# Kernel optimization log

Hardware: AMD Instinct MI355X
Metric: run time of the kernel (lower is better)

Reference implementation:

```python
import jax, jax.numpy as jnp
import numpy as np

B, S, D = 4, 2048, 1024
ATTN_D, OUT_D, H = 1024, 1024, 16
EPS = 1e-12


def setup_inputs() -> dict:
    key = jax.random.key(0)
    ks = jax.random.split(key, 9)
    s = 0.02
    return {
        "x": jax.random.normal(ks[0], (B, S, D), dtype=jnp.float32),
        "wq": jax.random.normal(ks[1], (D, ATTN_D), dtype=jnp.float32) * s,
        "bq": jnp.zeros((ATTN_D,), dtype=jnp.float32),
        "wk": jax.random.normal(ks[2], (D, ATTN_D), dtype=jnp.float32) * s,
        "bk": jnp.zeros((ATTN_D,), dtype=jnp.float32),
        "wv": jax.random.normal(ks[3], (D, ATTN_D), dtype=jnp.float32) * s,
        "bv": jnp.zeros((ATTN_D,), dtype=jnp.float32),
        "wo": jax.random.normal(ks[4], (ATTN_D, OUT_D), dtype=jnp.float32) * s,
        "bo": jnp.zeros((OUT_D,), dtype=jnp.float32),
        "ln_g": jnp.ones((OUT_D,), dtype=jnp.float32),
        "ln_b": jnp.zeros((OUT_D,), dtype=jnp.float32),
    }


def reference(x, wq, bq, wk, bk, wv, bv, wo, bo, ln_g, ln_b):
    b, s, _ = x.shape
    hd = ATTN_D // H  # head_dim
    # projections -> [B, H, S, hd]
    q = (x @ wq + bq).reshape(b, s, H, hd).transpose(0, 2, 1, 3)
    k = (x @ wk + bk).reshape(b, s, H, hd).transpose(0, 2, 1, 3)
    v = (x @ wv + bv).reshape(b, s, H, hd).transpose(0, 2, 1, 3)
    # full O(S^2) score matrix, as in the original module
    scores = jnp.einsum("bhqd,bhkd->bhqk", q, k) / jnp.sqrt(jnp.float32(hd))
    attn = jax.nn.softmax(scores, axis=-1)
    out = jnp.einsum("bhqk,bhkd->bhqd", attn, v)
    out = out.transpose(0, 2, 1, 3).reshape(b, s, ATTN_D)
    out = out @ wo + bo
    # LayerNorm (no residual in this module)
    mu = jnp.mean(out, axis=-1, keepdims=True)
    var = jnp.var(out, axis=-1, keepdims=True)
    out = (out - mu) * jax.lax.rsqrt(var + EPS) * ln_g + ln_b
    return out
```

## Files before the change

### kernel.cpp

```cpp
#include <hip/hip_runtime.h>

typedef __bf16 bf16;
typedef __bf16 bf16x4 __attribute__((ext_vector_type(4)));
typedef __bf16 bf16x8 __attribute__((ext_vector_type(8)));
typedef float f32x4 __attribute__((ext_vector_type(4)));

#define NB 4
#define NS 2048
#define ND 1024
#define NH 16
#define HD 64

#define QSCALE 0.18033688f

__device__ __forceinline__ void gload_lds16(const void* g, void* l) {
  __builtin_amdgcn_global_load_lds(
      (const __attribute__((address_space(1))) void*)g,
      (__attribute__((address_space(3))) void*)l, 16, 0, 0);
}

__device__ __forceinline__ float fast_exp2(float x) {
#if __has_builtin(__builtin_amdgcn_exp2f)
  return __builtin_amdgcn_exp2f(x);
#else
  return exp2f(x);
#endif
}

__global__ __launch_bounds__(256) void k_cvt(const float* __restrict__ src,
                                             bf16* __restrict__ dst) {
  size_t i = ((size_t)blockIdx.x * 256 + threadIdx.x) * 4;
  float4 v = *(const float4*)(src + i);
  bf16x4 o = {(__bf16)v.x, (__bf16)v.y, (__bf16)v.z, (__bf16)v.w};
  *(bf16x4*)(dst + i) = o;
}

__global__ __launch_bounds__(256) void k_cvt_T4(const float* __restrict__ wq,
                                                const float* __restrict__ wk,
                                                const float* __restrict__ wv,
                                                const float* __restrict__ wo,
                                                bf16* __restrict__ wqkvT,
                                                bf16* __restrict__ woT) {
  int z = blockIdx.z;
  const float* src = z == 0 ? wq : z == 1 ? wk : z == 2 ? wv : wo;
  bf16* dst = z < 3 ? wqkvT + (size_t)z * 1048576 : woT;
  __shared__ float t[32][33];
  int tx = threadIdx.x, ty = threadIdx.y;
  int x = blockIdx.x * 32 + tx;
  int y = blockIdx.y * 32 + ty;
#pragma unroll
  for (int j = 0; j < 4; ++j)
    t[ty + j * 8][tx] = src[(size_t)(y + j * 8) * 1024 + x];
  __syncthreads();
  int x2 = blockIdx.y * 32 + tx;
  int y2 = blockIdx.x * 32 + ty;
#pragma unroll
  for (int j = 0; j < 4; ++j)
    dst[(size_t)(y2 + j * 8) * 1024 + x2] = (__bf16)t[tx][ty + j * 8];
}

__global__ __launch_bounds__(256) void k_vT(const bf16* __restrict__ V,
                                            bf16* __restrict__ Vt) {
  __shared__ bf16 t[64][72];
  int tid = threadIdx.x;
  int bh = blockIdx.x >> 5, st = blockIdx.x & 31;
  int b = bh >> 4, h = bh & 15;
  const bf16* src = V + ((size_t)b * NS + st * 64) * ND + h * HD;
#pragma unroll
  for (int rep = 0; rep < 2; ++rep) {
    int idx = rep * 256 + tid;
    int r = idx >> 3, c8 = (idx & 7) * 8;
    *(bf16x8*)&t[r][c8] = *(const bf16x8*)(src + (size_t)r * ND + c8);
  }
  __syncthreads();
  bf16* dst = Vt + (size_t)bh * HD * NS + st * 64;
#pragma unroll
  for (int rep = 0; rep < 2; ++rep) {
    int idx = rep * 256 + tid;
    int d = idx >> 3, s8 = (idx & 7) * 8;
    bf16x8 v;
#pragma unroll
    for (int j = 0; j < 8; ++j) {
      int jj = (j + tid) & 7;
      v[jj] = t[s8 + jj][d];
    }
    *(bf16x8*)(dst + (size_t)d * NS + s8) = v;
  }
}

__device__ __forceinline__ void gemm256_mainloop(const bf16* __restrict__ A,
                                                 const bf16* __restrict__ BT,
                                                 int bm, int bn, bf16* As,
                                                 bf16* Bs, f32x4 acc[4][4]) {
  const int tid = threadIdx.x;
  const int w = tid >> 6, lane = tid & 63, quad = lane >> 4, l15 = lane & 15;
  const int l7 = l15 & 7, l8 = lane >> 3;
  const int wr = w >> 1, wc = w & 1;
  const int gsw = ((lane & 7) ^ l8) * 8;
  const bf16* gaw = A + (size_t)(bm * 256 + w * 8 + l8) * 1024 + gsw;
  const bf16* gbw = BT + (size_t)(bn * 128 + w * 8 + l8) * 1024 + gsw;
  bf16* daw = As + w * 512;
  bf16* dbw = Bs + w * 512;
  int aoff[4][2], boff[4][2];
#pragma unroll
  for (int mi = 0; mi < 4; ++mi)
#pragma unroll
    for (int ks = 0; ks < 2; ++ks)
      aoff[mi][ks] =
          (wr * 64 + mi * 16 + l15) * 64 + (((ks * 4 + quad) ^ l7) * 8);
#pragma unroll
  for (int ni = 0; ni < 4; ++ni)
#pragma unroll
    for (int ks = 0; ks < 2; ++ks)
      boff[ni][ks] =
          (wc * 64 + ni * 16 + l15) * 64 + (((ks * 4 + quad) ^ l7) * 8);

  auto stage = [&](int kt) {
    const int slot = kt % 3;
    const bf16* ga = gaw + kt * 64;
    const bf16* gb = gbw + kt * 64;
    bf16* da = daw + slot * 16384;
    bf16* db = dbw + slot * 8192;
#pragma unroll
    for (int ri = 0; ri < 4; ++ri)
      gload_lds16(ga + (size_t)(ri * 64) * 1024, da + ri * 4096);
#pragma unroll
    for (int ri = 0; ri < 2; ++ri)
      gload_lds16(gb + (size_t)(ri * 64) * 1024, db + ri * 4096);
  };

  stage(0);
  stage(1);
  asm volatile("s_waitcnt vmcnt(6)" ::: "memory");
  __builtin_amdgcn_s_barrier();

  for (int kt = 0; kt < 16; ++kt) {
    const int slot = kt % 3;
    if (kt + 2 < 16) stage(kt + 2);
    const bf16* a_ = As + slot * 16384;
    const bf16* b_ = Bs + slot * 8192;
    bf16x8 av[2][2], bv[4][2];
#pragma unroll
    for (int mi = 0; mi < 2; ++mi)
#pragma unroll
      for (int ks = 0; ks < 2; ++ks)
        av[mi][ks] = *(const bf16x8*)(a_ + aoff[mi][ks]);
#pragma unroll
    for (int ni = 0; ni < 4; ++ni)
#pragma unroll
      for (int ks = 0; ks < 2; ++ks)
        bv[ni][ks] = *(const bf16x8*)(b_ + boff[ni][ks]);
    __builtin_amdgcn_s_setprio(1);
#pragma unroll
    for (int mi = 0; mi < 2; ++mi)
#pragma unroll
      for (int ni = 0; ni < 4; ++ni)
#pragma unroll
        for (int ks = 0; ks < 2; ++ks)
          acc[mi][ni] = __builtin_amdgcn_mfma_f32_16x16x32_bf16(
              av[mi][ks], bv[ni][ks], acc[mi][ni], 0, 0, 0);
    __builtin_amdgcn_s_setprio(0);
    bf16x8 av2[2][2];
#pragma unroll
    for (int mi = 0; mi < 2; ++mi)
#pragma unroll
      for (int ks = 0; ks < 2; ++ks)
        av2[mi][ks] = *(const bf16x8*)(a_ + aoff[2 + mi][ks]);
    __builtin_amdgcn_s_setprio(1);
#pragma unroll
    for (int mi = 0; mi < 2; ++mi)
#pragma unroll
      for (int ni = 0; ni < 4; ++ni)
#pragma unroll
        for (int ks = 0; ks < 2; ++ks)
          acc[2 + mi][ni] = __builtin_amdgcn_mfma_f32_16x16x32_bf16(
              av2[mi][ks], bv[ni][ks], acc[2 + mi][ni], 0, 0, 0);
    __builtin_amdgcn_s_setprio(0);
    if (kt + 2 < 16)
      asm volatile("s_waitcnt vmcnt(6)" ::: "memory");
    else
      asm volatile("s_waitcnt vmcnt(0)" ::: "memory");
    if (kt + 1 < 16) __builtin_amdgcn_s_barrier();
  }
  __syncthreads();
}

__global__ __launch_bounds__(512, 2) void k_gemm_qkv(
    const bf16* __restrict__ A, const bf16* __restrict__ BT,
    const float* __restrict__ bq, const float* __restrict__ bk,
    const float* __restrict__ bv, bf16* __restrict__ Q, bf16* __restrict__ K,
    bf16* __restrict__ V) {
  __shared__ alignas(16) char smem[147456];
  bf16* As = (bf16*)smem;
  bf16* Bs = (bf16*)(smem + 98304);
  f32x4 acc[4][4] = {};
  const int bm = blockIdx.y, bn = blockIdx.x;
  gemm256_mainloop(A, BT, bm, bn, As, Bs, acc);
  const int tid = threadIdx.x;
  const int w = tid >> 6, lane = tid & 63, quad = lane >> 4, l15 = lane & 15;
  const int wr = w >> 1, wc = w & 1;
  bf16* sEw = (bf16*)smem + w * 4608;
  const int colbase = bn * 128 + wc * 64;
  const int which = colbase >> 10;
  const int nnbase = colbase & 1023;
  const float* bias = which == 0 ? bq : which == 1 ? bk : bv;
  bf16* dst = which == 0 ? Q : which == 1 ? K : V;
  const float scl = which == 0 ? QSCALE : 1.f;
  const int rowbase = bm * 256 + wr * 64;
#pragma unroll
  for (int ni = 0; ni < 4; ++ni) {
    float bb = bias[nnbase + ni * 16 + l15];
#pragma unroll
    for (int mi = 0; mi < 4; ++mi)
#pragma unroll
      for (int r = 0; r < 4; ++r)
        sEw[(mi * 16 + quad * 4 + r) * 72 + ni * 16 + l15] =
            (__bf16)((acc[mi][ni][r] + bb) * scl);
  }
  const int l8 = lane >> 3, g8 = (lane & 7) * 8;
#pragma unroll
  for (int i = 0; i < 8; ++i) {
    int row = i * 8 + l8;
    bf16x8 vv = *(const bf16x8*)(sEw + row * 72 + g8);
    *(bf16x8*)(dst + (size_t)(rowbase + row) * 1024 + nnbase + g8) = vv;
  }
}

__global__ __launch_bounds__(512, 2) void k_gemm_out(const bf16* __restrict__ A,
                                                     const bf16* __restrict__ BT,
                                                     const float* __restrict__ bo,
                                                     float* __restrict__ Y) {
  __shared__ alignas(16) char smem[147456];
  bf16* As = (bf16*)smem;
  bf16* Bs = (bf16*)(smem + 98304);
  f32x4 acc[4][4] = {};
  const int bm = blockIdx.y, bn = blockIdx.x;
  gemm256_mainloop(A, BT, bm, bn, As, Bs, acc);
  const int tid = threadIdx.x;
  const int w = tid >> 6, lane = tid & 63, quad = lane >> 4, l15 = lane & 15;
  const int wr = w >> 1, wc = w & 1;
  float* sEw = (float*)smem + w * 2176;
  const int colbase = bn * 128 + wc * 64;
  const int rowbase = bm * 256 + wr * 64;
  float bb[4];
#pragma unroll
  for (int ni = 0; ni < 4; ++ni) bb[ni] = bo[colbase + ni * 16 + l15];
  const int l4 = lane >> 4, c4 = (lane & 15) * 4;
#pragma unroll
  for (int h2 = 0; h2 < 2; ++h2) {
#pragma unroll
    for (int ml = 0; ml < 2; ++ml)
#pragma unroll
      for (int ni = 0; ni < 4; ++ni)
#pragma unroll
        for (int r = 0; r < 4; ++r)
          sEw[(ml * 16 + quad * 4 + r) * 68 + ni * 16 + l15] =
              acc[h2 * 2 + ml][ni][r] + bb[ni];
#pragma unroll
    for (int i = 0; i < 8; ++i) {
      int row = i * 4 + l4;
      float4 v = *(const float4*)(sEw + row * 68 + c4);
      *(float4*)(Y + (size_t)(rowbase + h2 * 32 + row) * 1024 + colbase + c4) =
          v;
    }
  }
}

__global__ __launch_bounds__(256, 4) void k_attn(const bf16* __restrict__ Qg,
                                                 const bf16* __restrict__ Kg,
                                                 const bf16* __restrict__ VtG,
                                                 bf16* __restrict__ O) {
  __shared__ alignas(16) char smem[40960];
  bf16* sK = (bf16*)smem;
  bf16* sVt = (bf16*)(smem + 16384);
  const int tid = threadIdx.x;
  const int w = tid >> 6, lane = tid & 63, quad = lane >> 4, l15 = lane & 15;
  const int l7 = l15 & 7, l8 = lane >> 3;
  const int sw = (l15 >> 1) & 3;
  const int bh = blockIdx.x & 63;
  const int qt = blockIdx.x >> 6;
  const int b = bh >> 4, h = bh & 15;
  const bf16* Qh = Qg + (size_t)b * NS * ND + h * HD;
  const bf16* Kh = Kg + (size_t)b * NS * ND + h * HD;
  const bf16* Vh = VtG + (size_t)bh * HD * NS;
  bf16* Pw = (bf16*)(smem + 32768) + w * 1024;

  const int q0 = qt * 128 + w * 32;
  bf16x8 qb[2][2];
#pragma unroll
  for (int ni = 0; ni < 2; ++ni)
#pragma unroll
    for (int ks = 0; ks < 2; ++ks)
      qb[ni][ks] = *(const bf16x8*)(Qh + (size_t)(q0 + ni * 16 + l15) * ND +
                                    ks * 32 + quad * 8);

  const int gsw = ((lane & 7) ^ l8) * 8;
  const bf16* gk = Kh + (size_t)(w * 8 + l8) * ND + gsw;
  const bf16* gv = Vh + (size_t)(w * 8 + l8) * NS + gsw;
  bf16* dk = sK + w * 512;
  bf16* dv = sVt + w * 512;

  f32x4 o_acc[4][2] = {};
  float l_run[2] = {0.f, 0.f};

  int offA[4][2];
#pragma unroll
  for (int mi = 0; mi < 4; ++mi)
#pragma unroll
    for (int ks = 0; ks < 2; ++ks)
      offA[mi][ks] = (mi * 16 + l15) * 64 + (((ks * 4 + quad) ^ l7) * 8);
  int offP[2], wbase[2], wg[2];
#pragma unroll
  for (int ni = 0; ni < 2; ++ni) {
    offP[ni] = (ni * 16 + l15) * 32 + ((quad ^ sw) * 8);
    wbase[ni] = (ni * 16 + l15) * 32 + (quad & 1) * 4;
  }
#pragma unroll
  for (int m2 = 0; m2 < 2; ++m2)
    wg[m2] = (((m2 * 2 + (quad >> 1)) ^ sw) * 8);

  gload_lds16(gk, dk);
  gload_lds16(gk + 32 * ND, dk + 2048);
  gload_lds16(gv, dv);
  gload_lds16(gv + 32 * NS, dv + 2048);

  for (int it = 0; it < NS / 64; ++it) {
    const int buf = (it & 1) * 4096;
    __syncthreads();
    if (it + 1 < NS / 64) {
      const int nbuf = 4096 - buf;
      const bf16* gk1 = gk + (size_t)(it + 1) * 64 * ND;
      const bf16* gv1 = gv + (it + 1) * 64;
      gload_lds16(gk1, dk + nbuf);
      gload_lds16(gk1 + 32 * ND, dk + nbuf + 2048);
      gload_lds16(gv1, dv + nbuf);
      gload_lds16(gv1 + 32 * NS, dv + nbuf + 2048);
    }

#pragma unroll
    for (int hf = 0; hf < 2; ++hf) {
#pragma unroll
      for (int m2 = 0; m2 < 2; ++m2) {
        const int mi = 2 * hf + m2;
        f32x4 s[2] = {};
#pragma unroll
        for (int ks = 0; ks < 2; ++ks) {
          bf16x8 ak = *(const bf16x8*)(sK + buf + offA[mi][ks]);
#pragma unroll
          for (int ni = 0; ni < 2; ++ni)
            s[ni] = __builtin_amdgcn_mfma_f32_16x16x32_bf16(ak, qb[ni][ks],
                                                            s[ni], 0, 0, 0);
        }
#pragma unroll
        for (int ni = 0; ni < 2; ++ni) {
#pragma unroll
          for (int r = 0; r < 4; ++r) {
            s[ni][r] = fast_exp2(s[ni][r]);
            l_run[ni] += s[ni][r];
          }
          bf16x4 p = {(__bf16)s[ni][0], (__bf16)s[ni][1], (__bf16)s[ni][2],
                      (__bf16)s[ni][3]};
          *(bf16x4*)(Pw + wbase[ni] + wg[m2]) = p;
        }
      }

      bf16x8 pb[2];
#pragma unroll
      for (int ni = 0; ni < 2; ++ni)
        pb[ni] = *(const bf16x8*)(Pw + offP[ni]);
#pragma unroll
      for (int mi = 0; mi < 4; ++mi) {
        bf16x8 av = *(const bf16x8*)(sVt + buf + offA[mi][hf]);
#pragma unroll
        for (int ni = 0; ni < 2; ++ni)
          o_acc[mi][ni] = __builtin_amdgcn_mfma_f32_16x16x32_bf16(
              av, pb[ni], o_acc[mi][ni], 0, 0, 0);
      }
    }
  }

#pragma unroll
  for (int ni = 0; ni < 2; ++ni) {
    float l = l_run[ni];
    l += __shfl_xor(l, 16, 64);
    l += __shfl_xor(l, 32, 64);
    float inv = 1.f / l;
    int q = q0 + ni * 16 + l15;
    size_t orow = ((size_t)b * NS + q) * 1024 + h * 64;
#pragma unroll
    for (int mi = 0; mi < 4; ++mi) {
      bf16x4 ov = {
          (__bf16)(o_acc[mi][ni][0] * inv), (__bf16)(o_acc[mi][ni][1] * inv),
          (__bf16)(o_acc[mi][ni][2] * inv), (__bf16)(o_acc[mi][ni][3] * inv)};
      *(bf16x4*)(O + orow + mi * 16 + quad * 4) = ov;
    }
  }
}

__global__ __launch_bounds__(256) void k_ln(float* __restrict__ Y,
                                            const float* __restrict__ g,
                                            const float* __restrict__ bta) {
  int row = blockIdx.x, tid = threadIdx.x;
  float4 v = ((const float4*)(Y + (size_t)row * 1024))[tid];
  float sm = v.x + v.y + v.z + v.w;
  float sq = v.x * v.x + v.y * v.y + v.z * v.z + v.w * v.w;
#pragma unroll
  for (int off = 1; off < 64; off <<= 1) {
    sm += __shfl_xor(sm, off, 64);
    sq += __shfl_xor(sq, off, 64);
  }
  __shared__ float red[8];
  int w = tid >> 6, lane = tid & 63;
  if (lane == 0) {
    red[w] = sm;
    red[4 + w] = sq;
  }
  __syncthreads();
  sm = red[0] + red[1] + red[2] + red[3];
  sq = red[4] + red[5] + red[6] + red[7];
  float mu = sm * (1.f / 1024.f);
  float var = sq * (1.f / 1024.f) - mu * mu;
  float rstd = rsqrtf(var + 1e-12f);
  float4 g4 = ((const float4*)g)[tid];
  float4 b4 = ((const float4*)bta)[tid];
  float4 o;
  o.x = (v.x - mu) * rstd * g4.x + b4.x;
  o.y = (v.y - mu) * rstd * g4.y + b4.y;
  o.z = (v.z - mu) * rstd * g4.z + b4.z;
  o.w = (v.w - mu) * rstd * g4.w + b4.w;
  ((float4*)(Y + (size_t)row * 1024))[tid] = o;
}

extern "C" void kernel_launch(void* const* d_in, const int* in_sizes, int n_in,
                              void* d_out, int out_size, void* d_ws,
                              size_t ws_size, hipStream_t stream) {
  const float* x = (const float*)d_in[0];
  const float* wq = (const float*)d_in[1];
  const float* bq = (const float*)d_in[2];
  const float* wk = (const float*)d_in[3];
  const float* bk = (const float*)d_in[4];
  const float* wv = (const float*)d_in[5];
  const float* bv = (const float*)d_in[6];
  const float* wo = (const float*)d_in[7];
  const float* bo = (const float*)d_in[8];
  const float* ln_g = (const float*)d_in[9];
  const float* ln_b = (const float*)d_in[10];
  float* out = (float*)d_out;

  char* ws = (char*)d_ws;
  bf16* xb = (bf16*)ws;          ws += 16777216;
  bf16* wqkvT = (bf16*)ws;       ws += 6291456;
  bf16* woT = (bf16*)ws;         ws += 2097152;
  bf16* Qh = (bf16*)ws;          ws += 16777216;
  bf16* Kh = (bf16*)ws;          ws += 16777216;
  bf16* Vh = (bf16*)ws;          ws += 16777216;
  bf16* Vt = (bf16*)ws;          ws += 16777216;
  bf16* AOb = (bf16*)ws;         ws += 16777216;

  k_cvt<<<8192, 256, 0, stream>>>(x, xb);
  dim3 tb(32, 8);
  k_cvt_T4<<<dim3(32, 32, 4), tb, 0, stream>>>(wq, wk, wv, wo, wqkvT, woT);

  k_gemm_qkv<<<dim3(24, 32), 512, 0, stream>>>(xb, wqkvT, bq, bk, bv, Qh, Kh,
                                               Vh);
  k_vT<<<NB * NH * 32, 256, 0, stream>>>(Vh, Vt);
  k_attn<<<NB * NH * (NS / 128), 256, 0, stream>>>(Qh, Kh, Vt, AOb);
  k_gemm_out<<<dim3(8, 32), 512, 0, stream>>>(AOb, woT, bo, out);
  k_ln<<<8192, 256, 0, stream>>>(out, ln_g, ln_b);
}
```

Measured before the change: 297.4 us.

## Fuse V transpose into QKV GEMM epilogue and split k-step into two phases

Drops the separate V-transpose kernel: the QKV GEMM epilogue now writes V straight into the transposed [B,H,D,S] layout from its LDS staging tile. This avoids one kernel launch and a full round trip of V through global memory. The GEMM main loop also changes. Each 64-wide k tile is now processed as two 32-wide halves, and global-to-LDS prefetch is split into two partial stages placed between them, with more barriers per iteration. The extra barriers may add synchronisation stalls, and the transposed epilogue writes are strided per row.

```diff
diff --git a/kernel.cpp b/kernel.cpp
--- a/kernel.cpp
+++ b/kernel.cpp
@@ -57,35 +57,6 @@
 #pragma unroll
   for (int j = 0; j < 4; ++j)
     dst[(size_t)(y2 + j * 8) * 1024 + x2] = (__bf16)t[tx][ty + j * 8];
-}
-
-__global__ __launch_bounds__(256) void k_vT(const bf16* __restrict__ V,
-                                            bf16* __restrict__ Vt) {
-  __shared__ bf16 t[64][72];
-  int tid = threadIdx.x;
-  int bh = blockIdx.x >> 5, st = blockIdx.x & 31;
-  int b = bh >> 4, h = bh & 15;
-  const bf16* src = V + ((size_t)b * NS + st * 64) * ND + h * HD;
-#pragma unroll
-  for (int rep = 0; rep < 2; ++rep) {
-    int idx = rep * 256 + tid;
-    int r = idx >> 3, c8 = (idx & 7) * 8;
-    *(bf16x8*)&t[r][c8] = *(const bf16x8*)(src + (size_t)r * ND + c8);
-  }
-  __syncthreads();
-  bf16* dst = Vt + (size_t)bh * HD * NS + st * 64;
-#pragma unroll
-  for (int rep = 0; rep < 2; ++rep) {
-    int idx = rep * 256 + tid;
-    int d = idx >> 3, s8 = (idx & 7) * 8;
-    bf16x8 v;
-#pragma unroll
-    for (int j = 0; j < 8; ++j) {
-      int jj = (j + tid) & 7;
-      v[jj] = t[s8 + jj][d];
-    }
-    *(bf16x8*)(dst + (size_t)d * NS + s8) = v;
-  }
 }
 
 __device__ __forceinline__ void gemm256_mainloop(const bf16* __restrict__ A,
@@ -115,72 +86,73 @@
       boff[ni][ks] =
           (wc * 64 + ni * 16 + l15) * 64 + (((ks * 4 + quad) ^ l7) * 8);
 
-  auto stage = [&](int kt) {
+  auto stageP0 = [&](int kt) {
+    const int slot = kt % 3;
+    const bf16* ga = gaw + kt * 64;
+    bf16* da = daw + slot * 16384;
+    gload_lds16(ga, da);
+    gload_lds16(ga + (size_t)64 * 1024, da + 4096);
+    gload_lds16(ga + (size_t)128 * 1024, da + 8192);
+  };
+  auto stageP1 = [&](int kt) {
     const int slot = kt % 3;
     const bf16* ga = gaw + kt * 64;
     const bf16* gb = gbw + kt * 64;
     bf16* da = daw + slot * 16384;
     bf16* db = dbw + slot * 8192;
-#pragma unroll
-    for (int ri = 0; ri < 4; ++ri)
-      gload_lds16(ga + (size_t)(ri * 64) * 1024, da + ri * 4096);
-#pragma unroll
-    for (int ri = 0; ri < 2; ++ri)
-      gload_lds16(gb + (size_t)(ri * 64) * 1024, db + ri * 4096);
+    gload_lds16(ga + (size_t)192 * 1024, da + 12288);
+    gload_lds16(gb, db);
+    gload_lds16(gb + (size_t)64 * 1024, db + 4096);
   };
 
-  stage(0);
-  stage(1);
+  stageP0(0);
+  stageP1(0);
+  stageP0(1);
+  stageP1(1);
   asm volatile("s_waitcnt vmcnt(6)" ::: "memory");
   __builtin_amdgcn_s_barrier();
 
   for (int kt = 0; kt < 16; ++kt) {
     const int slot = kt % 3;
-    if (kt + 2 < 16) stage(kt + 2);
     const bf16* a_ = As + slot * 16384;
     const bf16* b_ = Bs + slot * 8192;
-    bf16x8 av[2][2], bv[4][2];
-#pragma unroll
-    for (int mi = 0; mi < 2; ++mi)
-#pragma unroll
-      for (int ks = 0; ks < 2; ++ks)
-        av[mi][ks] = *(const bf16x8*)(a_ + aoff[mi][ks]);
-#pragma unroll
-    for (int ni = 0; ni < 4; ++ni)
-#pragma unroll
-      for (int ks = 0; ks < 2; ++ks)
-        bv[ni][ks] = *(const bf16x8*)(b_ + boff[ni][ks]);
+    bf16x8 av0[4], bv0[4];
+#pragma unroll
+    for (int i = 0; i < 4; ++i) av0[i] = *(const bf16x8*)(a_ + aoff[i][0]);
+#pragma unroll
+    for (int i = 0; i < 4; ++i) bv0[i] = *(const bf16x8*)(b_ + boff[i][0]);
+    if (kt + 2 < 16) stageP0(kt + 2);
+    __builtin_amdgcn_s_barrier();
     __builtin_amdgcn_s_setprio(1);
 #pragma unroll
-    for (int mi = 0; mi < 2; ++mi)
+    for (int mi = 0; mi < 4; ++mi)
 #pragma unroll
       for (int ni = 0; ni < 4; ++ni)
-#pragma unroll
-        for (int ks = 0; ks < 2; ++ks)
-          acc[mi][ni] = __builtin_amdgcn_mfma_f32_16x16x32_bf16(
-              av[mi][ks], bv[ni][ks], acc[mi][ni], 0, 0, 0);
+        acc[mi][ni] = __builtin_amdgcn_mfma_f32_16x16x32_bf16(
+            av0[mi], bv0[ni], acc[mi][ni], 0, 0, 0);
     __builtin_amdgcn_s_setprio(0);
-    bf16x8 av2[2][2];
-#pragma unroll
-    for (int mi = 0; mi < 2; ++mi)
-#pragma unroll
-      for (int ks = 0; ks < 2; ++ks)
-        av2[mi][ks] = *(const bf16x8*)(a_ + aoff[2 + mi][ks]);
+    __builtin_amdgcn_s_barrier();
+    bf16x8 av1[4], bv1[4];
+#pragma unroll
+    for (int i = 0; i < 4; ++i) av1[i] = *(const bf16x8*)(a_ + aoff[i][1]);
+#pragma unroll
+    for (int i = 0; i < 4; ++i) bv1[i] = *(const bf16x8*)(b_ + boff[i][1]);
+    if (kt + 2 < 16) {
+      stageP1(kt + 2);
+      asm volatile("s_waitcnt vmcnt(6)" ::: "memory");
+    } else if (kt + 1 < 16) {
+      asm volatile("s_waitcnt vmcnt(0)" ::: "memory");
+    }
+    __builtin_amdgcn_s_barrier();
     __builtin_amdgcn_s_setprio(1);
 #pragma unroll
-    for (int mi = 0; mi < 2; ++mi)
+    for (int mi = 0; mi < 4; ++mi)
 #pragma unroll
       for (int ni = 0; ni < 4; ++ni)
-#pragma unroll
-        for (int ks = 0; ks < 2; ++ks)
-          acc[2 + mi][ni] = __builtin_amdgcn_mfma_f32_16x16x32_bf16(
-              av2[mi][ks], bv[ni][ks], acc[2 + mi][ni], 0, 0, 0);
+        acc[mi][ni] = __builtin_amdgcn_mfma_f32_16x16x32_bf16(
+            av1[mi], bv1[ni], acc[mi][ni], 0, 0, 0);
     __builtin_amdgcn_s_setprio(0);
-    if (kt + 2 < 16)
-      asm volatile("s_waitcnt vmcnt(6)" ::: "memory");
-    else
-      asm volatile("s_waitcnt vmcnt(0)" ::: "memory");
-    if (kt + 1 < 16) __builtin_amdgcn_s_barrier();
+    __builtin_amdgcn_s_barrier();
   }
   __syncthreads();
 }
@@ -189,7 +161,7 @@
     const bf16* __restrict__ A, const bf16* __restrict__ BT,
     const float* __restrict__ bq, const float* __restrict__ bk,
     const float* __restrict__ bv, bf16* __restrict__ Q, bf16* __restrict__ K,
-    bf16* __restrict__ V) {
+    bf16* __restrict__ Vt) {
   __shared__ alignas(16) char smem[147456];
   bf16* As = (bf16*)smem;
   bf16* Bs = (bf16*)(smem + 98304);
@@ -204,7 +176,6 @@
   const int which = colbase >> 10;
   const int nnbase = colbase & 1023;
   const float* bias = which == 0 ? bq : which == 1 ? bk : bv;
-  bf16* dst = which == 0 ? Q : which == 1 ? K : V;
   const float scl = which == 0 ? QSCALE : 1.f;
   const int rowbase = bm * 256 + wr * 64;
 #pragma unroll
@@ -217,19 +188,39 @@
         sEw[(mi * 16 + quad * 4 + r) * 72 + ni * 16 + l15] =
             (__bf16)((acc[mi][ni][r] + bb) * scl);
   }
-  const int l8 = lane >> 3, g8 = (lane & 7) * 8;
-#pragma unroll
-  for (int i = 0; i < 8; ++i) {
-    int row = i * 8 + l8;
-    bf16x8 vv = *(const bf16x8*)(sEw + row * 72 + g8);
-    *(bf16x8*)(dst + (size_t)(rowbase + row) * 1024 + nnbase + g8) = vv;
-  }
-}
-
-__global__ __launch_bounds__(512, 2) void k_gemm_out(const bf16* __restrict__ A,
-                                                     const bf16* __restrict__ BT,
-                                                     const float* __restrict__ bo,
-                                                     float* __restrict__ Y) {
+  if (which < 2) {
+    bf16* dst = which == 0 ? Q : K;
+    const int l8 = lane >> 3, g8 = (lane & 7) * 8;
+#pragma unroll
+    for (int i = 0; i < 8; ++i) {
+      int row = i * 8 + l8;
+      bf16x8 vv = *(const bf16x8*)(sEw + row * 72 + g8);
+      *(bf16x8*)(dst + (size_t)(rowbase + row) * 1024 + nnbase + g8) = vv;
+    }
+  } else {
+    const int h = nnbase >> 6;
+    const int bq_ = rowbase >> 11;
+    const int s0 = rowbase & 2047;
+    bf16* dstT = Vt + (size_t)(bq_ * 16 + h) * 64 * NS + s0;
+    const int d = lane >> 3;
+    const int s8 = (lane & 7) * 8;
+#pragma unroll
+    for (int i = 0; i < 8; ++i) {
+      int dd = i * 8 + d;
+      bf16x8 v;
+#pragma unroll
+      for (int j = 0; j < 8; ++j) {
+        int jj = (j + lane) & 7;
+        v[jj] = sEw[(s8 + jj) * 72 + dd];
+      }
+      *(bf16x8*)(dstT + (size_t)dd * NS + s8) = v;
+    }
+  }
+}
+
+__global__ __launch_bounds__(512, 2) void k_gemm_out(
+    const bf16* __restrict__ A, const bf16* __restrict__ BT,
+    const float* __restrict__ bo, float* __restrict__ Y) {
   __shared__ alignas(16) char smem[147456];
   bf16* As = (bf16*)smem;
   bf16* Bs = (bf16*)(smem + 98304);
@@ -453,7 +444,6 @@
   bf16* woT = (bf16*)ws;         ws += 2097152;
   bf16* Qh = (bf16*)ws;          ws += 16777216;
   bf16* Kh = (bf16*)ws;          ws += 16777216;
-  bf16* Vh = (bf16*)ws;          ws += 16777216;
   bf16* Vt = (bf16*)ws;          ws += 16777216;
   bf16* AOb = (bf16*)ws;         ws += 16777216;
 
@@ -462,8 +452,7 @@
   k_cvt_T4<<<dim3(32, 32, 4), tb, 0, stream>>>(wq, wk, wv, wo, wqkvT, woT);
 
   k_gemm_qkv<<<dim3(24, 32), 512, 0, stream>>>(xb, wqkvT, bq, bk, bv, Qh, Kh,
-                                               Vh);
-  k_vT<<<NB * NH * 32, 256, 0, stream>>>(Vh, Vt);
+                                               Vt);
   k_attn<<<NB * NH * (NS / 128), 256, 0, stream>>>(Qh, Kh, Vt, AOb);
   k_gemm_out<<<dim3(8, 32), 512, 0, stream>>>(AOb, woT, bo, out);
   k_ln<<<8192, 256, 0, stream>>>(out, ln_g, ln_b);
```

After: 292.2 us. No clear change (-1.7%).
